# Optimization experiments

Measured on AMD Instinct MI355X. Metric: run time of the kernel, lower is better.

The kernel has to match this reference:

```python
import jax, jax.numpy as jnp
import numpy as np

B, N, H = 512, 100, 768
I = 2 * H  # intermediate_dim default = hidden_dim * 2
NUM_ANS = 16
MAX_ANS = 15
LN_EPS = 1e-5


def setup_inputs() -> dict:
    key = jax.random.key(0)
    ks = jax.random.split(key, 7)
    s = 0.02
    return {
        "v_emb": jax.random.normal(ks[0], (B, N, H), dtype=jnp.float32),
        "W1": jax.random.normal(ks[1], (H, I), dtype=jnp.float32) * s,
        "b1": jax.random.normal(ks[2], (I,), dtype=jnp.float32) * s,
        "gamma": jnp.ones((I,), dtype=jnp.float32),
        "beta": jnp.zeros((I,), dtype=jnp.float32),
        "W2": jax.random.normal(ks[3], (I, 1), dtype=jnp.float32) * s,
        "b2": jax.random.normal(ks[4], (1,), dtype=jnp.float32) * s,
    }


def reference(v_emb, W1, b1, gamma, beta, W2, b2):
    # Linear -> GELU (exact/erf, torch nn.GELU default) -> LayerNorm -> Linear
    h = jnp.einsum("bnh,hi->bni", v_emb, W1) + b1            # [B,N,I]
    h = jax.nn.gelu(h, approximate=False)
    mu = jnp.mean(h, axis=-1, keepdims=True)
    var = jnp.mean(jnp.square(h - mu), axis=-1, keepdims=True)
    h = (h - mu) * jax.lax.rsqrt(var + LN_EPS) * gamma + beta
    scores = jnp.einsum("bni,io->bno", h, W2) + b2           # [B,N,1]
    scores = jax.nn.sigmoid(scores)                           # sigmoid=True branch
    pred = jnp.sum(scores, axis=1)                            # [B,1]
    # pred_to_logits: vectorized round + clamp + one-hot scatter
    # str(int(round(p))) in {'0'..'15'} -> that id; negative -> 0; overflow -> max_ans
    aid = jnp.clip(jnp.round(pred[:, 0]).astype(jnp.int32), 0, MAX_ANS)
    logits = jax.nn.one_hot(aid, NUM_ANS, dtype=scores.dtype)  # [B,16]
    # original returns dict: scores, final_attention_map (==scores), pred, logits
    return scores, pred, logits
```

## Files before the change

kernel.cpp:

```cpp
#include <hip/hip_runtime.h>
#include <hip/hip_bf16.h>
#include <cstdint>
#include <cstddef>

#define BB   512
#define NN   100
#define HH   768
#define II   1536
#define MM   (BB*NN)

typedef __bf16 bf16;
typedef __bf16 bf16x4 __attribute__((ext_vector_type(4)));
typedef __bf16 bf16x8 __attribute__((ext_vector_type(8)));
typedef float  f32x4  __attribute__((ext_vector_type(4)));

__device__ __forceinline__ void gld_lds16(const bf16* g, bf16* l) {
    __builtin_amdgcn_global_load_lds(
        (const __attribute__((address_space(1))) void*)g,
        (__attribute__((address_space(3))) void*)l, 16, 0, 0);
}

template <int PAT>
__device__ __forceinline__ float swz_add(float x) {
    return x + __int_as_float(
        __builtin_amdgcn_ds_swizzle(__float_as_int(x), PAT));
}
__device__ __forceinline__ float red16(float x) {
    x = swz_add<0x041F>(x);
    x = swz_add<0x081F>(x);
    x = swz_add<0x101F>(x);
    x = swz_add<0x201F>(x);
    return x;
}

__device__ __forceinline__ float fast_gelu(float x) {
    const float ax = fabsf(x) * 0.70710678118654752f;
    const float t  = __builtin_amdgcn_rcpf(fmaf(0.3275911f, ax, 1.0f));
    float p = fmaf(1.061405429f, t, -1.453152027f);
    p = fmaf(p, t, 1.421413741f);
    p = fmaf(p, t, -0.284496736f);
    p = fmaf(p, t, 0.254829592f);
    p = p * t;
    const float e    = __expf(-ax * ax);
    const float erfa = fmaf(-p, e, 1.0f);
    const float erfx = copysignf(erfa, x);
    return 0.5f * x * (1.0f + erfx);
}

__global__ __launch_bounds__(256) void prep_kernel(
    const float* __restrict__ W1, const float* __restrict__ gamma,
    const float* __restrict__ beta, const float* __restrict__ W2,
    const float* __restrict__ b2,
    bf16* __restrict__ Wp, float* __restrict__ gw, float* __restrict__ scal)
{
    int bid = blockIdx.x;
    if (bid < 1152) {
        int t  = bid * 256 + threadIdx.x;
        int n  = t % II;
        int k0 = (t / II) * 4;
        bf16x4 v;
        v[0] = (bf16)W1[(size_t)(k0+0)*II + n];
        v[1] = (bf16)W1[(size_t)(k0+1)*II + n];
        v[2] = (bf16)W1[(size_t)(k0+2)*II + n];
        v[3] = (bf16)W1[(size_t)(k0+3)*II + n];
        *(bf16x4*)&Wp[(size_t)n*HH + k0] = v;
    } else if (bid == 1152) {
        for (int j = threadIdx.x; j < II; j += 256)
            gw[j] = gamma[j] * W2[j];
    } else {
        float s1 = 0.f, s2 = 0.f;
        for (int j = threadIdx.x; j < II; j += 256) {
            float w2 = W2[j];
            s1 += gamma[j] * w2;
            s2 += beta[j]  * w2;
        }
        #pragma unroll
        for (int off = 32; off; off >>= 1) {
            s1 += __shfl_down(s1, off, 64);
            s2 += __shfl_down(s2, off, 64);
        }
        __shared__ float a1[4], a2[4];
        int lane = threadIdx.x & 63, w = threadIdx.x >> 6;
        if (lane == 0) { a1[w] = s1; a2[w] = s2; }
        __syncthreads();
        if (threadIdx.x == 0) {
            scal[0] = a1[0] + a1[1] + a1[2] + a1[3];
            scal[1] = a2[0] + a2[1] + a2[2] + a2[3] + b2[0];
        }
    }
}

__global__ __launch_bounds__(256, 2) void gemm_part(
    const float* __restrict__ Af, const bf16* __restrict__ Wp,
    const float* __restrict__ b1, const float* __restrict__ gw,
    float* __restrict__ part)
{
    __shared__ bf16  As[2 * 128 * 32];
    __shared__ bf16  Bs[2 * 256 * 32];
    __shared__ float sred[2][128][3];

    const int tid  = threadIdx.x;
    const int lin  = (blockIdx.x & 7) * 300 + (blockIdx.x >> 3);
    const int mb   = lin / 6;
    const int nb   = lin % 6;
    const int lane = tid & 63;
    const int w    = tid >> 6;
    const int wm   = w >> 1;
    const int wn   = w & 1;
    const int m15  = lane & 15;
    const int q    = lane >> 4;
    const int row0 = mb * 128;

    const int r4   = lane >> 2;
    const int ksel = (lane & 3) ^ ((lane >> 3) & 3);
    const int kofs = ksel * 8;

    const float* aP = Af + (size_t)(row0    + w*32 + r4) * HH + kofs;
    const bf16*  bP = Wp + (size_t)(nb*256 + w*64 + r4) * HH + kofs;

    const int asW = w*1024 + lane*8;
    const int bsW = w*2048 + lane*8;
    const int xsel8 = ((q ^ ((m15 >> 1) & 3)) << 3);

    f32x4 acc[4][8] = {};

    #pragma unroll
    for (int it = 0; it < 4; ++it)
        gld_lds16(bP + (size_t)it*16*HH, &Bs[bsW + it*512]);
    {
        float4 p00 = *(const float4*)(aP);
        float4 p01 = *(const float4*)(aP + 4);
        float4 p10 = *(const float4*)(aP + 16*HH);
        float4 p11 = *(const float4*)(aP + 16*HH + 4);
        asm volatile("s_waitcnt vmcnt(0)" ::: "memory");
        bf16x8 o0 = { (bf16)p00.x,(bf16)p00.y,(bf16)p00.z,(bf16)p00.w,
                      (bf16)p01.x,(bf16)p01.y,(bf16)p01.z,(bf16)p01.w };
        bf16x8 o1 = { (bf16)p10.x,(bf16)p10.y,(bf16)p10.z,(bf16)p10.w,
                      (bf16)p11.x,(bf16)p11.y,(bf16)p11.z,(bf16)p11.w };
        *(bf16x8*)&As[asW]       = o0;
        *(bf16x8*)&As[asW + 512] = o1;
    }
    __syncthreads();

    for (int kt = 0; kt < 23; ++kt) {
        const int cur = kt & 1, nxt = cur ^ 1;

        const bf16*  bn = bP + (size_t)(kt + 1) * 32;
        const float* an = aP + (size_t)(kt + 1) * 32;
        #pragma unroll
        for (int it = 0; it < 4; ++it)
            gld_lds16(bn + (size_t)it*16*HH, &Bs[nxt*8192 + bsW + it*512]);
        float4 p00 = *(const float4*)(an);
        float4 p01 = *(const float4*)(an + 4);
        float4 p10 = *(const float4*)(an + 16*HH);
        float4 p11 = *(const float4*)(an + 16*HH + 4);

        bf16x8 af[4];
        #pragma unroll
        for (int mt = 0; mt < 4; ++mt)
            af[mt] = *(const bf16x8*)&As[cur*4096 + (wm*64 + mt*16 + m15)*32 + xsel8];
        #pragma unroll
        for (int nt = 0; nt < 8; ++nt) {
            bf16x8 bf = *(const bf16x8*)&Bs[cur*8192 + (wn*128 + nt*16 + m15)*32 + xsel8];
            #pragma unroll
            for (int mt = 0; mt < 4; ++mt)
                acc[mt][nt] = __builtin_amdgcn_mfma_f32_16x16x32_bf16(
                    af[mt], bf, acc[mt][nt], 0, 0, 0);
        }

        asm volatile("s_waitcnt vmcnt(0)" ::: "memory");
        {
            bf16x8 o0 = { (bf16)p00.x,(bf16)p00.y,(bf16)p00.z,(bf16)p00.w,
                          (bf16)p01.x,(bf16)p01.y,(bf16)p01.z,(bf16)p01.w };
            bf16x8 o1 = { (bf16)p10.x,(bf16)p10.y,(bf16)p10.z,(bf16)p10.w,
                          (bf16)p11.x,(bf16)p11.y,(bf16)p11.z,(bf16)p11.w };
            *(bf16x8*)&As[nxt*4096 + asW]       = o0;
            *(bf16x8*)&As[nxt*4096 + asW + 512] = o1;
        }
        __syncthreads();
    }
    {
        const int cur = 1;
        bf16x8 af[4];
        #pragma unroll
        for (int mt = 0; mt < 4; ++mt)
            af[mt] = *(const bf16x8*)&As[cur*4096 + (wm*64 + mt*16 + m15)*32 + xsel8];
        #pragma unroll
        for (int nt = 0; nt < 8; ++nt) {
            bf16x8 bf = *(const bf16x8*)&Bs[cur*8192 + (wn*128 + nt*16 + m15)*32 + xsel8];
            #pragma unroll
            for (int mt = 0; mt < 4; ++mt)
                acc[mt][nt] = __builtin_amdgcn_mfma_f32_16x16x32_bf16(
                    af[mt], bf, acc[mt][nt], 0, 0, 0);
        }
    }

    float bv[8], gv[8];
    #pragma unroll
    for (int nt = 0; nt < 8; ++nt) {
        const int col = nb*256 + wn*128 + nt*16 + m15;
        bv[nt] = b1[col];
        gv[nt] = gw[col];
    }

    #pragma unroll
    for (int mt = 0; mt < 4; ++mt) {
        #pragma unroll
        for (int r = 0; r < 4; ++r) {
            float x0 = 0.f, x1 = 0.f, x2 = 0.f;
            #pragma unroll
            for (int nt = 0; nt < 8; ++nt) {
                float g = fast_gelu(acc[mt][nt][r] + bv[nt]);
                x0 += g; x1 += g * g; x2 += g * gv[nt];
            }
            x0 = red16(x0); x1 = red16(x1); x2 = red16(x2);
            if (m15 == 0) {
                const int rl = wm*64 + mt*16 + q*4 + r;
                sred[wn][rl][0] = x0;
                sred[wn][rl][1] = x1;
                sred[wn][rl][2] = x2;
            }
        }
    }
    __syncthreads();

    if (tid < 128) {
        const size_t rg = (size_t)row0 + tid;
        #pragma unroll
        for (int s = 0; s < 3; ++s)
            part[(size_t)s * 6 * MM + (size_t)nb * MM + rg]
                = sred[0][tid][s] + sred[1][tid][s];
    }
}

__global__ __launch_bounds__(128) void score_pred(
    const float* __restrict__ part, const float* __restrict__ scal,
    float* __restrict__ o_scores, float* __restrict__ o_pred,
    float* __restrict__ o_logits)
{
    const int b = blockIdx.x, t = threadIdx.x;
    float s = 0.f;
    if (t < NN) {
        const size_t row = (size_t)b * NN + t;
        float Sh = 0.f, Shh = 0.f, Shg = 0.f;
        #pragma unroll
        for (int j = 0; j < 6; ++j) {
            Sh  += part[(size_t)0*6*MM + (size_t)j*MM + row];
            Shh += part[(size_t)1*6*MM + (size_t)j*MM + row];
            Shg += part[(size_t)2*6*MM + (size_t)j*MM + row];
        }
        const float mu   = Sh * (1.0f / II);
        const float var  = Shh * (1.0f / II) - mu * mu;
        const float rstd = rsqrtf(var + 1e-5f);
        const float z    = rstd * (Shg - mu * scal[0]) + scal[1];
        s = 1.0f / (1.0f + __expf(-z));
        o_scores[row] = s;
    }
    float v = s;
    #pragma unroll
    for (int off = 32; off; off >>= 1) v += __shfl_down(v, off, 64);
    __shared__ float ssum[2];
    const int lane = t & 63, w = t >> 6;
    if (lane == 0) ssum[w] = v;
    __syncthreads();
    const float p = ssum[0] + ssum[1];
    if (t == 0) o_pred[b] = p;
    if (t < 16) {
        int aid = (int)rintf(p);
        aid = aid < 0 ? 0 : (aid > 15 ? 15 : aid);
        o_logits[b * 16 + t] = (t == aid) ? 1.0f : 0.0f;
    }
}

extern "C" void kernel_launch(void* const* d_in, const int* in_sizes, int n_in,
                              void* d_out, int out_size, void* d_ws, size_t ws_size,
                              hipStream_t stream)
{
    const float* v_emb = (const float*)d_in[0];
    const float* W1    = (const float*)d_in[1];
    const float* b1    = (const float*)d_in[2];
    const float* gamma = (const float*)d_in[3];
    const float* beta  = (const float*)d_in[4];
    const float* W2    = (const float*)d_in[5];
    const float* b2    = (const float*)d_in[6];

    char* ws = (char*)d_ws;
    size_t off = 0;
    bf16*  Wp   = (bf16*)(ws + off);  off += (size_t)II * HH * 2;
    float* gw   = (float*)(ws + off); off += (size_t)II * 4;
    float* scal = (float*)(ws + off); off += 256;
    float* part = (float*)(ws + off); off += (size_t)MM * 18 * 4;

    float* out       = (float*)d_out;
    float* o_scores  = out;
    float* o_pred    = out + MM;
    float* o_logits  = out + MM + BB;

    hipLaunchKernelGGL(prep_kernel, dim3(1154), dim3(256), 0, stream,
                       W1, gamma, beta, W2, b2, Wp, gw, scal);
    hipLaunchKernelGGL(gemm_part, dim3((MM / 128) * 6), dim3(256),
                       0, stream, v_emb, Wp, b1, gw, part);
    hipLaunchKernelGGL(score_pred, dim3(BB), dim3(128), 0, stream,
                       part, scal, o_scores, o_pred, o_logits);
}
```

Measured before the change: 448.0 us.

## Pre-convert activations to swizzled bf16 and use 128x128 tiles with direct LDS loads

Adds a conversion pass that writes v_emb as pre-swizzled bf16 into workspace, so the GEMM can load both A and B through global_load_lds instead of register fp32 loads followed by conversion. The GEMM tile shrinks from 128x256 to 128x128, doubling the grid and the number of partial-sum columns that score_pred reduces. This removes in-loop conversion work and register staging. In exchange it adds an extra full read and write of the activation tensor (about 150MB of traffic) and re-reads A twelve times instead of six.

```diff
diff --git a/kernel.cpp b/kernel.cpp
--- a/kernel.cpp
+++ b/kernel.cpp
@@ -10,7 +10,6 @@
 #define MM   (BB*NN)
 
 typedef __bf16 bf16;
-typedef __bf16 bf16x4 __attribute__((ext_vector_type(4)));
 typedef __bf16 bf16x8 __attribute__((ext_vector_type(8)));
 typedef float  f32x4  __attribute__((ext_vector_type(4)));
 
@@ -47,24 +46,42 @@
     return 0.5f * x * (1.0f + erfx);
 }
 
-__global__ __launch_bounds__(256) void prep_kernel(
-    const float* __restrict__ W1, const float* __restrict__ gamma,
-    const float* __restrict__ beta, const float* __restrict__ W2,
-    const float* __restrict__ b2,
-    bf16* __restrict__ Wp, float* __restrict__ gw, float* __restrict__ scal)
-{
-    int bid = blockIdx.x;
-    if (bid < 1152) {
-        int t  = bid * 256 + threadIdx.x;
-        int n  = t % II;
-        int k0 = (t / II) * 4;
-        bf16x4 v;
-        v[0] = (bf16)W1[(size_t)(k0+0)*II + n];
-        v[1] = (bf16)W1[(size_t)(k0+1)*II + n];
-        v[2] = (bf16)W1[(size_t)(k0+2)*II + n];
-        v[3] = (bf16)W1[(size_t)(k0+3)*II + n];
-        *(bf16x4*)&Wp[(size_t)n*HH + k0] = v;
-    } else if (bid == 1152) {
+__global__ __launch_bounds__(256) void prep_conv(
+    const float* __restrict__ v, const float* __restrict__ W1,
+    const float* __restrict__ gamma, const float* __restrict__ beta,
+    const float* __restrict__ W2, const float* __restrict__ b2,
+    bf16* __restrict__ Av, bf16* __restrict__ Wp,
+    float* __restrict__ gw, float* __restrict__ scal)
+{
+    const int bid = blockIdx.x;
+    if (bid < 6400) {
+        const int r = threadIdx.x >> 5;
+        const int j = threadIdx.x & 31;
+        const size_t m = (size_t)bid * 8 + r;
+        const float* src = v + m * HH;
+        bf16* dst = Av + m * HH;
+        const int x = (int)((m >> 1) & 3);
+        #pragma unroll
+        for (int u = 0; u < 3; ++u) {
+            const int p = j * 3 + u;
+            const int g = (p & ~3) | ((p & 3) ^ x);
+            float4 a = *(const float4*)(src + g * 8);
+            float4 b = *(const float4*)(src + g * 8 + 4);
+            bf16x8 o = { (bf16)a.x,(bf16)a.y,(bf16)a.z,(bf16)a.w,
+                         (bf16)b.x,(bf16)b.y,(bf16)b.z,(bf16)b.w };
+            *(bf16x8*)(dst + p * 8) = o;
+        }
+    } else if (bid < 6976) {
+        const int t = (bid - 6400) * 256 + threadIdx.x;
+        const int n = t % II;
+        const int g = t / II;
+        const int p = (g & ~3) | ((g & 3) ^ ((n >> 1) & 3));
+        bf16x8 o;
+        #pragma unroll
+        for (int i = 0; i < 8; ++i)
+            o[i] = (bf16)W1[(size_t)(g * 8 + i) * II + n];
+        *(bf16x8*)&Wp[(size_t)n * HH + p * 8] = o;
+    } else if (bid == 6976) {
         for (int j = threadIdx.x; j < II; j += 256)
             gw[j] = gamma[j] * W2[j];
     } else {
@@ -90,19 +107,19 @@
     }
 }
 
-__global__ __launch_bounds__(256, 2) void gemm_part(
-    const float* __restrict__ Af, const bf16* __restrict__ Wp,
+__global__ __launch_bounds__(256) void gemm_part(
+    const bf16* __restrict__ Av, const bf16* __restrict__ Wp,
     const float* __restrict__ b1, const float* __restrict__ gw,
     float* __restrict__ part)
 {
-    __shared__ bf16  As[2 * 128 * 32];
-    __shared__ bf16  Bs[2 * 256 * 32];
+    __shared__ bf16  As[2][128 * 32];
+    __shared__ bf16  Bs[2][128 * 32];
     __shared__ float sred[2][128][3];
 
     const int tid  = threadIdx.x;
-    const int lin  = (blockIdx.x & 7) * 300 + (blockIdx.x >> 3);
-    const int mb   = lin / 6;
-    const int nb   = lin % 6;
+    const int lin  = (blockIdx.x & 7) * 600 + (blockIdx.x >> 3);
+    const int mb   = lin / 12;
+    const int nb   = lin % 12;
     const int lane = tid & 63;
     const int w    = tid >> 6;
     const int wm   = w >> 1;
@@ -111,94 +128,68 @@
     const int q    = lane >> 4;
     const int row0 = mb * 128;
 
-    const int r4   = lane >> 2;
-    const int ksel = (lane & 3) ^ ((lane >> 3) & 3);
-    const int kofs = ksel * 8;
-
-    const float* aP = Af + (size_t)(row0    + w*32 + r4) * HH + kofs;
-    const bf16*  bP = Wp + (size_t)(nb*256 + w*64 + r4) * HH + kofs;
-
-    const int asW = w*1024 + lane*8;
-    const int bsW = w*2048 + lane*8;
-    const int xsel8 = ((q ^ ((m15 >> 1) & 3)) << 3);
-
-    f32x4 acc[4][8] = {};
-
-    #pragma unroll
-    for (int it = 0; it < 4; ++it)
-        gld_lds16(bP + (size_t)it*16*HH, &Bs[bsW + it*512]);
-    {
-        float4 p00 = *(const float4*)(aP);
-        float4 p01 = *(const float4*)(aP + 4);
-        float4 p10 = *(const float4*)(aP + 16*HH);
-        float4 p11 = *(const float4*)(aP + 16*HH + 4);
-        asm volatile("s_waitcnt vmcnt(0)" ::: "memory");
-        bf16x8 o0 = { (bf16)p00.x,(bf16)p00.y,(bf16)p00.z,(bf16)p00.w,
-                      (bf16)p01.x,(bf16)p01.y,(bf16)p01.z,(bf16)p01.w };
-        bf16x8 o1 = { (bf16)p10.x,(bf16)p10.y,(bf16)p10.z,(bf16)p10.w,
-                      (bf16)p11.x,(bf16)p11.y,(bf16)p11.z,(bf16)p11.w };
-        *(bf16x8*)&As[asW]       = o0;
-        *(bf16x8*)&As[asW + 512] = o1;
-    }
+    const int srow = tid >> 2;
+    const int sc   = tid & 3;
+    const bf16* aP = Av + (size_t)(row0     + srow) * HH + sc * 8;
+    const bf16* bP = Wp + (size_t)(nb * 128 + srow) * HH + sc * 8;
+    bf16* asD = &As[0][0] + tid * 8;
+    bf16* bsD = &Bs[0][0] + tid * 8;
+
+    const int xsel = (q ^ ((m15 >> 1) & 3)) * 8;
+
+    f32x4 acc[4][4] = {};
+
+    gld_lds16(aP,           asD);
+    gld_lds16(aP + 64 * HH, asD + 2048);
+    gld_lds16(bP,           bsD);
+    gld_lds16(bP + 64 * HH, bsD + 2048);
+    asm volatile("s_waitcnt vmcnt(0)" ::: "memory");
     __syncthreads();
 
     for (int kt = 0; kt < 23; ++kt) {
         const int cur = kt & 1, nxt = cur ^ 1;
-
-        const bf16*  bn = bP + (size_t)(kt + 1) * 32;
-        const float* an = aP + (size_t)(kt + 1) * 32;
-        #pragma unroll
-        for (int it = 0; it < 4; ++it)
-            gld_lds16(bn + (size_t)it*16*HH, &Bs[nxt*8192 + bsW + it*512]);
-        float4 p00 = *(const float4*)(an);
-        float4 p01 = *(const float4*)(an + 4);
-        float4 p10 = *(const float4*)(an + 16*HH);
-        float4 p11 = *(const float4*)(an + 16*HH + 4);
+        const int ko  = (kt + 1) * 32;
+
+        gld_lds16(aP + ko,           asD + nxt * 4096);
+        gld_lds16(aP + ko + 64 * HH, asD + nxt * 4096 + 2048);
+        gld_lds16(bP + ko,           bsD + nxt * 4096);
+        gld_lds16(bP + ko + 64 * HH, bsD + nxt * 4096 + 2048);
 
         bf16x8 af[4];
         #pragma unroll
         for (int mt = 0; mt < 4; ++mt)
-            af[mt] = *(const bf16x8*)&As[cur*4096 + (wm*64 + mt*16 + m15)*32 + xsel8];
-        #pragma unroll
-        for (int nt = 0; nt < 8; ++nt) {
-            bf16x8 bf = *(const bf16x8*)&Bs[cur*8192 + (wn*128 + nt*16 + m15)*32 + xsel8];
+            af[mt] = *(const bf16x8*)&As[cur][(wm*64 + mt*16 + m15)*32 + xsel];
+        #pragma unroll
+        for (int nt = 0; nt < 4; ++nt) {
+            bf16x8 bfr = *(const bf16x8*)&Bs[cur][(wn*64 + nt*16 + m15)*32 + xsel];
             #pragma unroll
             for (int mt = 0; mt < 4; ++mt)
                 acc[mt][nt] = __builtin_amdgcn_mfma_f32_16x16x32_bf16(
-                    af[mt], bf, acc[mt][nt], 0, 0, 0);
+                    af[mt], bfr, acc[mt][nt], 0, 0, 0);
         }
 
         asm volatile("s_waitcnt vmcnt(0)" ::: "memory");
-        {
-            bf16x8 o0 = { (bf16)p00.x,(bf16)p00.y,(bf16)p00.z,(bf16)p00.w,
-                          (bf16)p01.x,(bf16)p01.y,(bf16)p01.z,(bf16)p01.w };
-            bf16x8 o1 = { (bf16)p10.x,(bf16)p10.y,(bf16)p10.z,(bf16)p10.w,
-                          (bf16)p11.x,(bf16)p11.y,(bf16)p11.z,(bf16)p11.w };
-            *(bf16x8*)&As[nxt*4096 + asW]       = o0;
-            *(bf16x8*)&As[nxt*4096 + asW + 512] = o1;
-        }
         __syncthreads();
     }
     {
-        const int cur = 1;
         bf16x8 af[4];
         #pragma unroll
         for (int mt = 0; mt < 4; ++mt)
-            af[mt] = *(const bf16x8*)&As[cur*4096 + (wm*64 + mt*16 + m15)*32 + xsel8];
-        #pragma unroll
-        for (int nt = 0; nt < 8; ++nt) {
-            bf16x8 bf = *(const bf16x8*)&Bs[cur*8192 + (wn*128 + nt*16 + m15)*32 + xsel8];
+            af[mt] = *(const bf16x8*)&As[1][(wm*64 + mt*16 + m15)*32 + xsel];
+        #pragma unroll
+        for (int nt = 0; nt < 4; ++nt) {
+            bf16x8 bfr = *(const bf16x8*)&Bs[1][(wn*64 + nt*16 + m15)*32 + xsel];
             #pragma unroll
             for (int mt = 0; mt < 4; ++mt)
                 acc[mt][nt] = __builtin_amdgcn_mfma_f32_16x16x32_bf16(
-                    af[mt], bf, acc[mt][nt], 0, 0, 0);
-        }
-    }
-
-    float bv[8], gv[8];
+                    af[mt], bfr, acc[mt][nt], 0, 0, 0);
+        }
+    }
+
+    float bv[4], gv[4];
     #pragma unroll
-    for (int nt = 0; nt < 8; ++nt) {
-        const int col = nb*256 + wn*128 + nt*16 + m15;
+    for (int nt = 0; nt < 4; ++nt) {
+        const int col = nb*128 + wn*64 + nt*16 + m15;
         bv[nt] = b1[col];
         gv[nt] = gw[col];
     }
@@ -209,7 +200,7 @@
         for (int r = 0; r < 4; ++r) {
             float x0 = 0.f, x1 = 0.f, x2 = 0.f;
             #pragma unroll
-            for (int nt = 0; nt < 8; ++nt) {
+            for (int nt = 0; nt < 4; ++nt) {
                 float g = fast_gelu(acc[mt][nt][r] + bv[nt]);
                 x0 += g; x1 += g * g; x2 += g * gv[nt];
             }
@@ -228,7 +219,7 @@
         const size_t rg = (size_t)row0 + tid;
         #pragma unroll
         for (int s = 0; s < 3; ++s)
-            part[(size_t)s * 6 * MM + (size_t)nb * MM + rg]
+            part[(size_t)s * 12 * MM + (size_t)nb * MM + rg]
                 = sred[0][tid][s] + sred[1][tid][s];
     }
 }
@@ -244,10 +235,10 @@
         const size_t row = (size_t)b * NN + t;
         float Sh = 0.f, Shh = 0.f, Shg = 0.f;
         #pragma unroll
-        for (int j = 0; j < 6; ++j) {
-            Sh  += part[(size_t)0*6*MM + (size_t)j*MM + row];
-            Shh += part[(size_t)1*6*MM + (size_t)j*MM + row];
-            Shg += part[(size_t)2*6*MM + (size_t)j*MM + row];
+        for (int j = 0; j < 12; ++j) {
+            Sh  += part[(size_t)0*12*MM + (size_t)j*MM + row];
+            Shh += part[(size_t)1*12*MM + (size_t)j*MM + row];
+            Shg += part[(size_t)2*12*MM + (size_t)j*MM + row];
         }
         const float mu   = Sh * (1.0f / II);
         const float var  = Shh * (1.0f / II) - mu * mu;
@@ -289,17 +280,18 @@
     bf16*  Wp   = (bf16*)(ws + off);  off += (size_t)II * HH * 2;
     float* gw   = (float*)(ws + off); off += (size_t)II * 4;
     float* scal = (float*)(ws + off); off += 256;
-    float* part = (float*)(ws + off); off += (size_t)MM * 18 * 4;
+    float* part = (float*)(ws + off); off += (size_t)MM * 36 * 4;
+    bf16*  Av   = (bf16*)(ws + off);  off += (size_t)MM * HH * 2;
 
     float* out       = (float*)d_out;
     float* o_scores  = out;
     float* o_pred    = out + MM;
     float* o_logits  = out + MM + BB;
 
-    hipLaunchKernelGGL(prep_kernel, dim3(1154), dim3(256), 0, stream,
-                       W1, gamma, beta, W2, b2, Wp, gw, scal);
-    hipLaunchKernelGGL(gemm_part, dim3((MM / 128) * 6), dim3(256),
-                       0, stream, v_emb, Wp, b1, gw, part);
+    hipLaunchKernelGGL(prep_conv, dim3(6978), dim3(256), 0, stream,
+                       v_emb, W1, gamma, beta, W2, b2, Av, Wp, gw, scal);
+    hipLaunchKernelGGL(gemm_part, dim3((MM / 128) * 12), dim3(256),
+                       0, stream, Av, Wp, b1, gw, part);
     hipLaunchKernelGGL(score_pred, dim3(BB), dim3(128), 0, stream,
                        part, scal, o_scores, o_pred, o_logits);
 }
```

After: 422.7 us. 5.7% less time.
